# Kernel tuning notes

Measured on AMD Instinct MI355X. Metric: run time of the kernel, lower is better.

Reference implementation:

```python
import jax, jax.numpy as jnp
import numpy as np

FDIM, HDIM, DIM = 512, 512, 256
B, N = 64, 4096


def setup_inputs() -> dict:
    key = jax.random.key(0)
    k1, k2, k3, k4, k5 = jax.random.split(key, 5)
    image_features = jax.random.normal(k1, (B, N, FDIM), dtype=jnp.float32)
    hidden_state = jax.random.normal(k2, (B, HDIM), dtype=jnp.float32)
    # nn.Linear weights: stored [out, in]; y = x @ W.T
    W_img = jax.random.normal(k3, (DIM, FDIM), dtype=jnp.float32) * (FDIM ** -0.5)
    W_hid = jax.random.normal(k4, (DIM, HDIM), dtype=jnp.float32) * (HDIM ** -0.5)
    W_score = jax.random.normal(k5, (1, DIM), dtype=jnp.float32) * (DIM ** -0.5)
    return {"image_features": image_features, "hidden_state": hidden_state,
            "W_img": W_img, "W_hid": W_hid, "W_score": W_score}


def reference(image_features, hidden_state, W_img, W_hid, W_score):
    # proj_image: [B, N, D]
    proj_image = jnp.einsum('bnf,df->bnd', image_features, W_img)
    # proj_hidden: [B, 1, D]
    proj_hidden = jnp.einsum('bh,dh->bd', hidden_state, W_hid)[:, None, :]
    combined = jnp.tanh(proj_image + proj_hidden)            # [B, N, D]
    scores = jnp.einsum('bnd,d->bn', combined, W_score[0])   # [B, N]
    weights = jax.nn.softmax(scores, axis=-1)                # [B, N]
    context = jnp.einsum('bn,bnf->bf', weights, image_features)  # [B, F]
    return (context, weights)
```

## Files before the change

kernel.cpp:

```cpp
#include <hip/hip_runtime.h>
#include <hip/hip_bf16.h>

#define B_ 64
#define N_ 4096
#define F_ 512
#define D_ 256
#define BM 32
#define BK 64
#define APAD 520
#define NCHUNK (N_ / BM)
#define NBLK (B_ * NCHUNK)

typedef __attribute__((ext_vector_type(8))) short short8;
typedef __attribute__((ext_vector_type(4))) float f32x4;

__device__ __forceinline__ unsigned short f2bf(float f) {
  unsigned int u = __float_as_uint(f);
  u += 0x7FFFu + ((u >> 16) & 1u);
  return (unsigned short)(u >> 16);
}

__device__ __forceinline__ unsigned int pk2bf(float x, float y) {
  float2 f; f.x = x; f.y = y;
  __hip_bfloat162 h = __float22bfloat162_rn(f);
  union { __hip_bfloat162 h2; unsigned int u; } cv; cv.h2 = h;
  return cv.u;
}

__device__ __forceinline__ float fast_tanh(float x) {
  float e = __expf(-2.0f * fabsf(x));
  float t = (1.0f - e) / (1.0f + e);
  return copysignf(t, x);
}

__global__ void prep_w_kernel(const float* __restrict__ Wimg,
                              unsigned short* __restrict__ wfrag) {
  int d = blockIdx.x;
  int f = threadIdx.x;
  int kt = f >> 6, ks = (f >> 5) & 1, lg = (f >> 3) & 3, e = f & 7;
  int lr = d & 15, d16 = d >> 4;
  int lane = lg * 16 + lr;
  int idx = (((kt * 2 + ks) * 16 + d16) * 64 + lane) * 8 + e;
  wfrag[idx] = f2bf(Wimg[d * F_ + f]);
}

__global__ void prep_ph_kernel(const float* __restrict__ hid,
                               const float* __restrict__ Whid,
                               float* __restrict__ ph) {
  int b = blockIdx.x, d = threadIdx.x;
  const float4* hv = (const float4*)(hid + b * F_);
  const float4* wv = (const float4*)(Whid + d * F_);
  float acc = 0.f;
#pragma unroll 4
  for (int i = 0; i < 128; i++) {
    float4 h = hv[i], w = wv[i];
    acc += h.x * w.x + h.y * w.y + h.z * w.z + h.w * w.w;
  }
  ph[b * D_ + d] = acc;
}

__global__ __launch_bounds__(256, 4) void fused_kernel(
    const float* __restrict__ feat, const unsigned short* __restrict__ wfrag,
    const float* __restrict__ ph, const float* __restrict__ wscore,
    float* __restrict__ expw, float2* __restrict__ meta,
    float* __restrict__ part) {
  __shared__ unsigned short Afull[BM * APAD];
  __shared__ float red[BM][4];
  __shared__ float sbuf[BM];
  __shared__ float ewf[BM];

  int tid = threadIdx.x;
  int lane = tid & 63, wn = tid >> 6;
  int lr = lane & 15, lg = lane >> 4;

  int blk = blockIdx.x;
  int b = blk >> 7, chunk = blk & 127;
  int n0 = chunk * BM;

  const float* arow = feat + (size_t)(b * N_ + n0) * F_;

  f32x4 acc[2][4];
#pragma unroll
  for (int m = 0; m < 2; m++)
#pragma unroll
    for (int n = 0; n < 4; n++) acc[m][n] = (f32x4)0.f;

  int r_[2], c4_[2];
#pragma unroll
  for (int i = 0; i < 2; i++) {
    int idx4 = tid + i * 256;
    r_[i] = idx4 >> 4;
    c4_[i] = idx4 & 15;
  }

#define LOADA(buf, kt_)                                                        \
  _Pragma("unroll") for (int i = 0; i < 2; i++)                                \
      buf[i] = *(const float4*)(arow + (size_t)r_[i] * F_ + (kt_)*BK + c4_[i] * 4);

#define CVTWRITE(buf, kt_)                                                     \
  _Pragma("unroll") for (int i = 0; i < 2; i++) {                              \
    unsigned int p0 = pk2bf(buf[i].x, buf[i].y);                               \
    unsigned int p1 = pk2bf(buf[i].z, buf[i].w);                               \
    *(uint2*)(Afull + r_[i] * APAD + (kt_)*BK + c4_[i] * 4) = make_uint2(p0, p1); \
  }

#define MFMASTEP(kt_)                                                          \
  _Pragma("unroll") for (int ks = 0; ks < 2; ks++) {                           \
    short8 bfr[4], af[2];                                                      \
    _Pragma("unroll") for (int n = 0; n < 4; n++)                              \
        bfr[n] = *(const short8*)(wfrag +                                      \
            (size_t)((((kt_)*2 + ks) * 16 + wn * 4 + n) * 64 + lane) * 8);     \
    _Pragma("unroll") for (int m = 0; m < 2; m++)                              \
        af[m] = *(const short8*)(Afull + (m * 16 + lr) * APAD + (kt_)*BK + ks * 32 + lg * 8); \
    _Pragma("unroll") for (int m = 0; m < 2; m++)                              \
      _Pragma("unroll") for (int n = 0; n < 4; n++)                            \
        acc[m][n] = __builtin_amdgcn_mfma_f32_16x16x32_bf16(af[m], bfr[n], acc[m][n], 0, 0, 0); \
  }

  float4 rA[2], rB[2];
  LOADA(rA, 0);
  LOADA(rB, 1);
  CVTWRITE(rA, 0);
  __syncthreads();

#pragma unroll
  for (int kt = 0; kt < 8; kt += 2) {
    if (kt + 2 < 8) { LOADA(rA, kt + 2); }
    MFMASTEP(kt);
    CVTWRITE(rB, kt + 1);
    __syncthreads();
    if (kt + 3 < 8) { LOADA(rB, kt + 3); }
    MFMASTEP(kt + 1);
    if (kt + 2 < 8) { CVTWRITE(rA, kt + 2); }
    __syncthreads();
  }

  float ph4[4], wv4[4];
#pragma unroll
  for (int n = 0; n < 4; n++) {
    int d = wn * 64 + n * 16 + lr;
    ph4[n] = ph[b * D_ + d];
    wv4[n] = wscore[d];
  }
#pragma unroll
  for (int m = 0; m < 2; m++) {
#pragma unroll
    for (int j = 0; j < 4; j++) {
      float p = 0.f;
#pragma unroll
      for (int n = 0; n < 4; n++)
        p += fast_tanh(acc[m][n][j] + ph4[n]) * wv4[n];
      p += __shfl_xor(p, 1);
      p += __shfl_xor(p, 2);
      p += __shfl_xor(p, 4);
      p += __shfl_xor(p, 8);
      if (lr == 0) red[m * 16 + lg * 4 + j][wn] = p;
    }
  }
  __syncthreads();
  if (tid < BM) sbuf[tid] = red[tid][0] + red[tid][1] + red[tid][2] + red[tid][3];
  __syncthreads();

  float mb = -1e30f;
#pragma unroll
  for (int r = 0; r < BM; r++) mb = fmaxf(mb, sbuf[r]);
  if (tid < BM) {
    float e = __expf(sbuf[tid] - mb);
    ewf[tid] = e;
    expw[b * N_ + n0 + tid] = e;
    float l = e;
#pragma unroll
    for (int o = 1; o < 32; o <<= 1) l += __shfl_xor(l, o);
    if (tid == 0) meta[blk] = make_float2(mb, l);
  }
  __syncthreads();

  int f0 = tid * 2;
  float a0 = 0.f, a1 = 0.f;
#pragma unroll 8
  for (int r = 0; r < BM; r++) {
    float w = ewf[r];
    unsigned int v = *(const unsigned int*)(Afull + r * APAD + f0);
    a0 += w * __uint_as_float(v << 16);
    a1 += w * __uint_as_float(v & 0xffff0000u);
  }
  float2 o; o.x = a0; o.y = a1;
  *(float2*)(part + (size_t)blk * F_ + f0) = o;
}

__global__ void finalize_kernel(const float* __restrict__ part,
                                const float2* __restrict__ meta,
                                const float* __restrict__ expw,
                                float* __restrict__ ctx,
                                float* __restrict__ wout) {
  __shared__ float sm[NCHUNK], sl[NCHUNK], se[NCHUNK];
  int b = blockIdx.x, t = threadIdx.x;
  if (t < NCHUNK) {
    float2 ml = meta[b * NCHUNK + t];
    sm[t] = ml.x;
    sl[t] = ml.y;
  }
  __syncthreads();
  float M = -1e30f;
#pragma unroll 8
  for (int i = 0; i < NCHUNK; i++) M = fmaxf(M, sm[i]);
  float Z = 0.f;
#pragma unroll 8
  for (int i = 0; i < NCHUNK; i++) Z += sl[i] * __expf(sm[i] - M);
  if (t < NCHUNK) se[t] = __expf(sm[t] - M);
  __syncthreads();
  float invZ = 1.0f / Z;
  float acc = 0.f;
#pragma unroll 8
  for (int i = 0; i < NCHUNK; i++) acc += part[(size_t)(b * NCHUNK + i) * F_ + t] * se[i];
  ctx[b * F_ + t] = acc * invZ;
#pragma unroll
  for (int k = 0; k < 8; k++) {
    int n = k * 512 + t;
    wout[b * N_ + n] = expw[b * N_ + n] * se[n >> 5] * invZ;
  }
}

extern "C" void kernel_launch(void* const* d_in, const int* in_sizes, int n_in,
                              void* d_out, int out_size, void* d_ws, size_t ws_size,
                              hipStream_t stream) {
  const float* feat   = (const float*)d_in[0];
  const float* hid    = (const float*)d_in[1];
  const float* Wimg   = (const float*)d_in[2];
  const float* Whid   = (const float*)d_in[3];
  const float* Wscore = (const float*)d_in[4];

  float* ctx  = (float*)d_out;
  float* wout = (float*)d_out + B_ * F_;

  unsigned short* wfrag = (unsigned short*)d_ws;
  float*  ph    = (float*)((char*)d_ws + 262144);
  float*  expw  = (float*)((char*)d_ws + 327680);
  float2* meta  = (float2*)((char*)d_ws + 1376256);
  float*  part  = (float*)((char*)d_ws + 1441792);

  prep_w_kernel<<<D_, F_, 0, stream>>>(Wimg, wfrag);
  prep_ph_kernel<<<B_, D_, 0, stream>>>(hid, Whid, ph);
  fused_kernel<<<NBLK, 256, 0, stream>>>(feat, wfrag, ph, Wscore, expw, meta, part);
  finalize_kernel<<<B_, 512, 0, stream>>>(part, meta, expw, ctx, wout);
}
```

Before: 212.8 us.

## Restructure A-tile pipeline into 128-wide phases with B-fragment double buffering

Switches the feature-tile staging from 64-wide double-buffered register chunks to four 128-column phases, each with one global load, convert and LDS write, and one barrier per phase. This halves the number of barriers. Weight fragments are now software-pipelined: the next group's loads are issued before the current group's MFMAs, and s_setprio raises wave priority around the MFMA bursts. The weight fragment layout index is simplified to match. The cost is more live registers (four float4 A loads plus two sets of B fragments), which may pressure occupancy under launch_bounds(256,4).

```diff
diff --git a/kernel.cpp b/kernel.cpp
--- a/kernel.cpp
+++ b/kernel.cpp
@@ -6,7 +6,6 @@
 #define F_ 512
 #define D_ 256
 #define BM 32
-#define BK 64
 #define APAD 520
 #define NCHUNK (N_ / BM)
 #define NBLK (B_ * NCHUNK)
@@ -37,10 +36,10 @@
                               unsigned short* __restrict__ wfrag) {
   int d = blockIdx.x;
   int f = threadIdx.x;
-  int kt = f >> 6, ks = (f >> 5) & 1, lg = (f >> 3) & 3, e = f & 7;
+  int q = f >> 5, lg = (f >> 3) & 3, e = f & 7;
   int lr = d & 15, d16 = d >> 4;
   int lane = lg * 16 + lr;
-  int idx = (((kt * 2 + ks) * 16 + d16) * 64 + lane) * 8 + e;
+  int idx = ((q * 16 + d16) * 64 + lane) * 8 + e;
   wfrag[idx] = f2bf(Wimg[d * F_ + f]);
 }
 
@@ -85,55 +84,87 @@
 #pragma unroll
     for (int n = 0; n < 4; n++) acc[m][n] = (f32x4)0.f;
 
-  int r_[2], c4_[2];
-#pragma unroll
-  for (int i = 0; i < 2; i++) {
+  int r2_[4], c4_[4];
+#pragma unroll
+  for (int i = 0; i < 4; i++) {
     int idx4 = tid + i * 256;
-    r_[i] = idx4 >> 4;
-    c4_[i] = idx4 & 15;
-  }
-
-#define LOADA(buf, kt_)                                                        \
-  _Pragma("unroll") for (int i = 0; i < 2; i++)                                \
-      buf[i] = *(const float4*)(arow + (size_t)r_[i] * F_ + (kt_)*BK + c4_[i] * 4);
-
-#define CVTWRITE(buf, kt_)                                                     \
-  _Pragma("unroll") for (int i = 0; i < 2; i++) {                              \
-    unsigned int p0 = pk2bf(buf[i].x, buf[i].y);                               \
-    unsigned int p1 = pk2bf(buf[i].z, buf[i].w);                               \
-    *(uint2*)(Afull + r_[i] * APAD + (kt_)*BK + c4_[i] * 4) = make_uint2(p0, p1); \
-  }
-
-#define MFMASTEP(kt_)                                                          \
-  _Pragma("unroll") for (int ks = 0; ks < 2; ks++) {                           \
-    short8 bfr[4], af[2];                                                      \
-    _Pragma("unroll") for (int n = 0; n < 4; n++)                              \
-        bfr[n] = *(const short8*)(wfrag +                                      \
-            (size_t)((((kt_)*2 + ks) * 16 + wn * 4 + n) * 64 + lane) * 8);     \
-    _Pragma("unroll") for (int m = 0; m < 2; m++)                              \
-        af[m] = *(const short8*)(Afull + (m * 16 + lr) * APAD + (kt_)*BK + ks * 32 + lg * 8); \
-    _Pragma("unroll") for (int m = 0; m < 2; m++)                              \
-      _Pragma("unroll") for (int n = 0; n < 4; n++)                            \
-        acc[m][n] = __builtin_amdgcn_mfma_f32_16x16x32_bf16(af[m], bfr[n], acc[m][n], 0, 0, 0); \
-  }
-
-  float4 rA[2], rB[2];
-  LOADA(rA, 0);
-  LOADA(rB, 1);
-  CVTWRITE(rA, 0);
-  __syncthreads();
-
-#pragma unroll
-  for (int kt = 0; kt < 8; kt += 2) {
-    if (kt + 2 < 8) { LOADA(rA, kt + 2); }
-    MFMASTEP(kt);
-    CVTWRITE(rB, kt + 1);
-    __syncthreads();
-    if (kt + 3 < 8) { LOADA(rB, kt + 3); }
-    MFMASTEP(kt + 1);
-    if (kt + 2 < 8) { CVTWRITE(rA, kt + 2); }
-    __syncthreads();
-  }
+    r2_[i] = idx4 >> 5;
+    c4_[i] = idx4 & 31;
+  }
+
+  float4 ra[4];
+
+#define LOADA2(p_)                                                             \
+  _Pragma("unroll") for (int i = 0; i < 4; i++)                                \
+      ra[i] = *(const float4*)(arow + (size_t)r2_[i] * F_ + (p_)*128 + c4_[i] * 4);
+
+#define CVT2(p_)                                                               \
+  _Pragma("unroll") for (int i = 0; i < 4; i++) {                              \
+    unsigned int p0 = pk2bf(ra[i].x, ra[i].y);                                 \
+    unsigned int p1 = pk2bf(ra[i].z, ra[i].w);                                 \
+    *(uint2*)(Afull + r2_[i] * APAD + (p_)*128 + c4_[i] * 4) = make_uint2(p0, p1); \
+  }
+
+#define BGRP(dst, q_)                                                          \
+  _Pragma("unroll") for (int n = 0; n < 4; n++)                                \
+      dst[n] = *(const short8*)(wfrag + (size_t)(((q_)*16 + wn * 4 + n) * 64 + lane) * 8);
+
+#define GRPMFMA(bsrc, q_)                                                      \
+  {                                                                            \
+    short8 af0 = *(const short8*)(Afull + lr * APAD + (q_)*32 + lg * 8);       \
+    short8 af1 = *(const short8*)(Afull + (16 + lr) * APAD + (q_)*32 + lg * 8);\
+    _Pragma("unroll") for (int n = 0; n < 4; n++) {                            \
+      acc[0][n] = __builtin_amdgcn_mfma_f32_16x16x32_bf16(af0, bsrc[n], acc[0][n], 0, 0, 0); \
+      acc[1][n] = __builtin_amdgcn_mfma_f32_16x16x32_bf16(af1, bsrc[n], acc[1][n], 0, 0, 0); \
+    }                                                                          \
+  }
+
+  short8 bf0[4], bf1[4];
+
+  LOADA2(0);
+  CVT2(0);
+  __syncthreads();
+
+  LOADA2(1);
+  BGRP(bf0, 0);
+  __builtin_amdgcn_s_setprio(1);
+  BGRP(bf1, 1); GRPMFMA(bf0, 0);
+  BGRP(bf0, 2); GRPMFMA(bf1, 1);
+  BGRP(bf1, 3); GRPMFMA(bf0, 2);
+  GRPMFMA(bf1, 3);
+  __builtin_amdgcn_s_setprio(0);
+  CVT2(1);
+  __syncthreads();
+
+  LOADA2(2);
+  BGRP(bf0, 4);
+  __builtin_amdgcn_s_setprio(1);
+  BGRP(bf1, 5); GRPMFMA(bf0, 4);
+  BGRP(bf0, 6); GRPMFMA(bf1, 5);
+  BGRP(bf1, 7); GRPMFMA(bf0, 6);
+  GRPMFMA(bf1, 7);
+  __builtin_amdgcn_s_setprio(0);
+  CVT2(2);
+  __syncthreads();
+
+  LOADA2(3);
+  BGRP(bf0, 8);
+  __builtin_amdgcn_s_setprio(1);
+  BGRP(bf1, 9);  GRPMFMA(bf0, 8);
+  BGRP(bf0, 10); GRPMFMA(bf1, 9);
+  BGRP(bf1, 11); GRPMFMA(bf0, 10);
+  GRPMFMA(bf1, 11);
+  __builtin_amdgcn_s_setprio(0);
+  CVT2(3);
+  __syncthreads();
+
+  BGRP(bf0, 12);
+  __builtin_amdgcn_s_setprio(1);
+  BGRP(bf1, 13); GRPMFMA(bf0, 12);
+  BGRP(bf0, 14); GRPMFMA(bf1, 13);
+  BGRP(bf1, 15); GRPMFMA(bf0, 14);
+  GRPMFMA(bf1, 15);
+  __builtin_amdgcn_s_setprio(0);
 
   float ph4[4], wv4[4];
 #pragma unroll
```

After: 218.7 us. 2.8% more time.

## Warp-specialize fused kernel into producer and MFMA consumer waves

Applied to the files above, without the earlier changes.

Doubles the block to 512 threads. Four producer waves load fp32 features, convert them to bf16 and write 128-column phases into LDS. Four consumer waves run the MFMA GEMM on the previous phase, with explicit sched barriers and s_barrier between phases. The W fragment layout is flattened to a single k-quarter index to match. The aim is to overlap global loads and conversion with matrix math, at the cost of fewer blocks per CU and half the waves sitting idle in each role.

```diff
diff --git a/kernel.cpp b/kernel.cpp
--- a/kernel.cpp
+++ b/kernel.cpp
@@ -6,7 +6,6 @@
 #define F_ 512
 #define D_ 256
 #define BM 32
-#define BK 64
 #define APAD 520
 #define NCHUNK (N_ / BM)
 #define NBLK (B_ * NCHUNK)
@@ -33,14 +32,27 @@
   return copysignf(t, x);
 }
 
+#define SBAR                                                                   \
+  do {                                                                         \
+    __builtin_amdgcn_sched_barrier(0);                                         \
+    __builtin_amdgcn_s_barrier();                                              \
+    __builtin_amdgcn_sched_barrier(0);                                         \
+  } while (0)
+
+#define LGKM0                                                                  \
+  do {                                                                         \
+    asm volatile("s_waitcnt lgkmcnt(0)" ::: "memory");                         \
+    __builtin_amdgcn_sched_barrier(0);                                         \
+  } while (0)
+
 __global__ void prep_w_kernel(const float* __restrict__ Wimg,
                               unsigned short* __restrict__ wfrag) {
   int d = blockIdx.x;
   int f = threadIdx.x;
-  int kt = f >> 6, ks = (f >> 5) & 1, lg = (f >> 3) & 3, e = f & 7;
+  int q = f >> 5, lg = (f >> 3) & 3, e = f & 7;
   int lr = d & 15, d16 = d >> 4;
   int lane = lg * 16 + lr;
-  int idx = (((kt * 2 + ks) * 16 + d16) * 64 + lane) * 8 + e;
+  int idx = ((q * 16 + d16) * 64 + lane) * 8 + e;
   wfrag[idx] = f2bf(Wimg[d * F_ + f]);
 }
 
@@ -59,7 +71,7 @@
   ph[b * D_ + d] = acc;
 }
 
-__global__ __launch_bounds__(256, 4) void fused_kernel(
+__global__ __launch_bounds__(512, 2) void fused_kernel(
     const float* __restrict__ feat, const unsigned short* __restrict__ wfrag,
     const float* __restrict__ ph, const float* __restrict__ wscore,
     float* __restrict__ expw, float2* __restrict__ meta,
@@ -70,8 +82,10 @@
   __shared__ float ewf[BM];
 
   int tid = threadIdx.x;
-  int lane = tid & 63, wn = tid >> 6;
+  int lane = tid & 63, wid = tid >> 6;
   int lr = lane & 15, lg = lane >> 4;
+  bool prod = (wid < 4);
+  int cw = prod ? 0 : (wid - 4);
 
   int blk = blockIdx.x;
   int b = blk >> 7, chunk = blk & 127;
@@ -79,82 +93,81 @@
 
   const float* arow = feat + (size_t)(b * N_ + n0) * F_;
 
-  f32x4 acc[2][4];
-#pragma unroll
-  for (int m = 0; m < 2; m++)
-#pragma unroll
-    for (int n = 0; n < 4; n++) acc[m][n] = (f32x4)0.f;
-
-  int r_[2], c4_[2];
-#pragma unroll
-  for (int i = 0; i < 2; i++) {
-    int idx4 = tid + i * 256;
-    r_[i] = idx4 >> 4;
-    c4_[i] = idx4 & 15;
-  }
-
-#define LOADA(buf, kt_)                                                        \
-  _Pragma("unroll") for (int i = 0; i < 2; i++)                                \
-      buf[i] = *(const float4*)(arow + (size_t)r_[i] * F_ + (kt_)*BK + c4_[i] * 4);
-
-#define CVTWRITE(buf, kt_)                                                     \
-  _Pragma("unroll") for (int i = 0; i < 2; i++) {                              \
+  f32x4 acc0[4], acc1[4];
+#pragma unroll
+  for (int n = 0; n < 4; n++) { acc0[n] = (f32x4)0.f; acc1[n] = (f32x4)0.f; }
+
+  int ptid = tid & 255;
+  int r2_[4], c4_[4];
+#pragma unroll
+  for (int i = 0; i < 4; i++) {
+    int idx4 = ptid + i * 256;
+    r2_[i] = idx4 >> 5;
+    c4_[i] = idx4 & 31;
+  }
+  float4 ra0[4], ra1[4];
+
+#define LOADA(buf, p_)                                                         \
+  _Pragma("unroll") for (int i = 0; i < 4; i++)                                \
+      buf[i] = *(const float4*)(arow + (size_t)r2_[i] * F_ + (p_)*128 + c4_[i] * 4);
+
+#define CVT(buf, p_)                                                           \
+  _Pragma("unroll") for (int i = 0; i < 4; i++) {                              \
     unsigned int p0 = pk2bf(buf[i].x, buf[i].y);                               \
     unsigned int p1 = pk2bf(buf[i].z, buf[i].w);                               \
-    *(uint2*)(Afull + r_[i] * APAD + (kt_)*BK + c4_[i] * 4) = make_uint2(p0, p1); \
-  }
-
-#define MFMASTEP(kt_)                                                          \
-  _Pragma("unroll") for (int ks = 0; ks < 2; ks++) {                           \
-    short8 bfr[4], af[2];                                                      \
+    *(uint2*)(Afull + r2_[i] * APAD + (p_)*128 + c4_[i] * 4) = make_uint2(p0, p1); \
+  }
+
+  const unsigned short* bbase = wfrag + (size_t)((cw * 4) * 64 + lane) * 8;
+
+#define QSTEP(q_)                                                              \
+  {                                                                            \
+    short8 bf[4];                                                              \
     _Pragma("unroll") for (int n = 0; n < 4; n++)                              \
-        bfr[n] = *(const short8*)(wfrag +                                      \
-            (size_t)((((kt_)*2 + ks) * 16 + wn * 4 + n) * 64 + lane) * 8);     \
-    _Pragma("unroll") for (int m = 0; m < 2; m++)                              \
-        af[m] = *(const short8*)(Afull + (m * 16 + lr) * APAD + (kt_)*BK + ks * 32 + lg * 8); \
-    _Pragma("unroll") for (int m = 0; m < 2; m++)                              \
-      _Pragma("unroll") for (int n = 0; n < 4; n++)                            \
-        acc[m][n] = __builtin_amdgcn_mfma_f32_16x16x32_bf16(af[m], bfr[n], acc[m][n], 0, 0, 0); \
-  }
-
-  float4 rA[2], rB[2];
-  LOADA(rA, 0);
-  LOADA(rB, 1);
-  CVTWRITE(rA, 0);
-  __syncthreads();
-
-#pragma unroll
-  for (int kt = 0; kt < 8; kt += 2) {
-    if (kt + 2 < 8) { LOADA(rA, kt + 2); }
-    MFMASTEP(kt);
-    CVTWRITE(rB, kt + 1);
-    __syncthreads();
-    if (kt + 3 < 8) { LOADA(rB, kt + 3); }
-    MFMASTEP(kt + 1);
-    if (kt + 2 < 8) { CVTWRITE(rA, kt + 2); }
-    __syncthreads();
-  }
-
-  float ph4[4], wv4[4];
-#pragma unroll
-  for (int n = 0; n < 4; n++) {
-    int d = wn * 64 + n * 16 + lr;
-    ph4[n] = ph[b * D_ + d];
-    wv4[n] = wscore[d];
-  }
-#pragma unroll
-  for (int m = 0; m < 2; m++) {
-#pragma unroll
-    for (int j = 0; j < 4; j++) {
-      float p = 0.f;
-#pragma unroll
-      for (int n = 0; n < 4; n++)
-        p += fast_tanh(acc[m][n][j] + ph4[n]) * wv4[n];
-      p += __shfl_xor(p, 1);
-      p += __shfl_xor(p, 2);
-      p += __shfl_xor(p, 4);
-      p += __shfl_xor(p, 8);
-      if (lr == 0) red[m * 16 + lg * 4 + j][wn] = p;
+        bf[n] = *(const short8*)(bbase + (size_t)(((q_)*16 + n) * 64) * 8);    \
+    short8 a0 = *(const short8*)(Afull + lr * APAD + (q_)*32 + lg * 8);        \
+    short8 a1 = *(const short8*)(Afull + (16 + lr) * APAD + (q_)*32 + lg * 8); \
+    _Pragma("unroll") for (int n = 0; n < 4; n++) {                            \
+      acc0[n] = __builtin_amdgcn_mfma_f32_16x16x32_bf16(a0, bf[n], acc0[n], 0, 0, 0); \
+      acc1[n] = __builtin_amdgcn_mfma_f32_16x16x32_bf16(a1, bf[n], acc1[n], 0, 0, 0); \
+    }                                                                          \
+  }
+
+#define PHASE(p_) { QSTEP((p_)*4+0); QSTEP((p_)*4+1); QSTEP((p_)*4+2); QSTEP((p_)*4+3); }
+
+  if (prod) { LOADA(ra0, 0); LOADA(ra1, 1); CVT(ra0, 0); LGKM0; }
+  SBAR;
+  if (prod) { LOADA(ra0, 2); CVT(ra1, 1); LGKM0; } else { PHASE(0); }
+  SBAR;
+  if (prod) { LOADA(ra1, 3); CVT(ra0, 2); LGKM0; } else { PHASE(1); }
+  SBAR;
+  if (prod) { CVT(ra1, 3); LGKM0; } else { PHASE(2); }
+  SBAR;
+  if (!prod) {
+    PHASE(3);
+    float ph4[4], wv4[4];
+#pragma unroll
+    for (int n = 0; n < 4; n++) {
+      int d = cw * 64 + n * 16 + lr;
+      ph4[n] = ph[b * D_ + d];
+      wv4[n] = wscore[d];
+    }
+#pragma unroll
+    for (int m = 0; m < 2; m++) {
+#pragma unroll
+      for (int j = 0; j < 4; j++) {
+        float p = 0.f;
+#pragma unroll
+        for (int n = 0; n < 4; n++) {
+          float v = (m == 0) ? acc0[n][j] : acc1[n][j];
+          p += fast_tanh(v + ph4[n]) * wv4[n];
+        }
+        p += __shfl_xor(p, 1);
+        p += __shfl_xor(p, 2);
+        p += __shfl_xor(p, 4);
+        p += __shfl_xor(p, 8);
+        if (lr == 0) red[m * 16 + lg * 4 + j][cw] = p;
+      }
     }
   }
   __syncthreads();
@@ -175,17 +188,19 @@
   }
   __syncthreads();
 
-  int f0 = tid * 2;
-  float a0 = 0.f, a1 = 0.f;
-#pragma unroll 8
-  for (int r = 0; r < BM; r++) {
-    float w = ewf[r];
-    unsigned int v = *(const unsigned int*)(Afull + r * APAD + f0);
-    a0 += w * __uint_as_float(v << 16);
-    a1 += w * __uint_as_float(v & 0xffff0000u);
-  }
-  float2 o; o.x = a0; o.y = a1;
-  *(float2*)(part + (size_t)blk * F_ + f0) = o;
+  if (tid < 256) {
+    int f0 = tid * 2;
+    float a0 = 0.f, a1 = 0.f;
+#pragma unroll 8
+    for (int r = 0; r < BM; r++) {
+      float w = ewf[r];
+      unsigned int v = *(const unsigned int*)(Afull + r * APAD + f0);
+      a0 += w * __uint_as_float(v << 16);
+      a1 += w * __uint_as_float(v & 0xffff0000u);
+    }
+    float2 o; o.x = a0; o.y = a1;
+    *(float2*)(part + (size_t)blk * F_ + f0) = o;
+  }
 }
 
 __global__ void finalize_kernel(const float* __restrict__ part,
@@ -241,6 +256,6 @@
 
   prep_w_kernel<<<D_, F_, 0, stream>>>(Wimg, wfrag);
   prep_ph_kernel<<<B_, D_, 0, stream>>>(hid, Whid, ph);
-  fused_kernel<<<NBLK, 256, 0, stream>>>(feat, wfrag, ph, Wscore, expw, meta, part);
+  fused_kernel<<<NBLK, 512, 0, stream>>>(feat, wfrag, ph, Wscore, expw, meta, part);
   finalize_kernel<<<B_, 512, 0, stream>>>(part, meta, expw, ctx, wout);
 }
```

Measured after the change: 281.6 us. +32.3%, slower.
